# Performance work log

Hardware: AMD Instinct MI355X
Metric: run time of the kernel (lower is better)

Reference implementation:

```python
import jax, jax.numpy as jnp
import numpy as np

PI = 3.141592653589793
EPS = 1e-12  # torch.nn.functional.normalize default eps


def setup_inputs() -> dict:
    key = jax.random.key(0)
    k1, k2, k3, k4 = jax.random.split(key, 4)
    N, D, E, R = 100000, 128, 640000, 500
    z = jax.random.normal(k1, (N, D), dtype=jnp.float32)
    edge_index = jax.random.randint(k2, (2, E), 0, N, dtype=jnp.int64)
    edge_type = jax.random.randint(k3, (E,), 0, R, dtype=jnp.int64)
    # learned relation phases, init uniform(-pi, pi) as in reset_parameters
    phase_rel = jax.random.uniform(k4, (R, D), dtype=jnp.float32, minval=-PI, maxval=PI)
    return {"z": z, "edge_index": edge_index, "edge_type": edge_type, "phase_rel": phase_rel}


def reference(z, edge_index, edge_type, phase_rel):
    # L2-normalize node embeddings along feature dim (torch F.normalize semantics)
    norm = jnp.sqrt(jnp.sum(z * z, axis=1, keepdims=True))
    z = z / jnp.maximum(norm, EPS)
    # z is real (imaginary part zero), rel = exp(i * phase).
    # Re( z_src * rel * conj(z_dst) ) with real z_src, z_dst reduces to
    # z_src * cos(phase) * z_dst  (the sin term multiplies a zero imaginary part).
    z_src = z[edge_index[0]]              # [E, D]
    z_dst = z[edge_index[1]]              # [E, D]
    cos_p = jnp.cos(phase_rel)[edge_type]  # [E, D]
    return jnp.sum(z_src * cos_p * z_dst, axis=1)  # [E]
```

## Files before the change

kernel.cpp:

```cpp
#include <hip/hip_runtime.h>
#include <math.h>

#define D 128
#define EPS_NORM 1e-12f

__device__ __forceinline__ unsigned int f32_to_bf16(float f) {
    unsigned int u = __float_as_uint(f);
    return (u + 0x7FFFu + ((u >> 16) & 1u)) >> 16;
}
__device__ __forceinline__ float bf_lo(unsigned int w) { return __uint_as_float(w << 16); }
__device__ __forceinline__ float bf_hi(unsigned int w) { return __uint_as_float(w & 0xFFFF0000u); }

__global__ void norm_pack_kernel(const float* __restrict__ z,
                                 unsigned int* __restrict__ zn, int N) {
    int w    = blockIdx.x * (blockDim.x >> 6) + (threadIdx.x >> 6);
    int lane = threadIdx.x & 63;
    int half = lane >> 5;
    int hl   = lane & 31;
    int row  = w * 2 + half;
    if (row >= N) return;
    float4 v = reinterpret_cast<const float4*>(z + (size_t)row * D)[hl];
    float s = v.x * v.x + v.y * v.y + v.z * v.z + v.w * v.w;
#pragma unroll
    for (int off = 16; off > 0; off >>= 1) s += __shfl_xor(s, off, 32);
    float inv = 1.0f / fmaxf(sqrtf(s), EPS_NORM);
    uint2 o;
    o.x = (f32_to_bf16(v.y * inv) << 16) | f32_to_bf16(v.x * inv);
    o.y = (f32_to_bf16(v.w * inv) << 16) | f32_to_bf16(v.z * inv);
    reinterpret_cast<uint2*>(zn + (size_t)row * (D / 2))[hl] = o;
}

__global__ void cos_pack_kernel(const float* __restrict__ phase,
                                unsigned int* __restrict__ ct, int n2) {
    int i = blockIdx.x * blockDim.x + threadIdx.x;
    if (i < n2) {
        float a = cosf(phase[2 * i]);
        float b = cosf(phase[2 * i + 1]);
        ct[i] = (f32_to_bf16(b) << 16) | f32_to_bf16(a);
    }
}

__device__ __forceinline__ float dot8(uint4 sw, uint4 cw, uint4 dw) {
    float p;
    p = bf_lo(sw.x) * bf_lo(cw.x) * bf_lo(dw.x);
    p = fmaf(bf_hi(sw.x) * bf_hi(cw.x), bf_hi(dw.x), p);
    p = fmaf(bf_lo(sw.y) * bf_lo(cw.y), bf_lo(dw.y), p);
    p = fmaf(bf_hi(sw.y) * bf_hi(cw.y), bf_hi(dw.y), p);
    p = fmaf(bf_lo(sw.z) * bf_lo(cw.z), bf_lo(dw.z), p);
    p = fmaf(bf_hi(sw.z) * bf_hi(cw.z), bf_hi(dw.z), p);
    p = fmaf(bf_lo(sw.w) * bf_lo(cw.w), bf_lo(dw.w), p);
    p = fmaf(bf_hi(sw.w) * bf_hi(cw.w), bf_hi(dw.w), p);
    return p;
}

__global__ __launch_bounds__(256, 6) void edge_kernel_v4(
    const unsigned int* __restrict__ zn,
    const unsigned int* __restrict__ ct,
    const int* __restrict__ ei,
    const int* __restrict__ et,
    float* __restrict__ out, int E) {
    const uint4* zn4 = reinterpret_cast<const uint4*>(zn);
    const uint4* ct4 = reinterpret_cast<const uint4*>(ct);
    int tid     = (int)(blockIdx.x * blockDim.x + threadIdx.x);
    int gid     = tid >> 4;
    int l       = threadIdx.x & 15;
    int ngroups = (int)((gridDim.x * blockDim.x) >> 4);
    int stride  = ngroups * 4;
    int E4      = E & ~3;

    int e = gid * 4;
    int s0, s1, s2, s3, d0, d1, d2, d3, t0, t1, t2, t3;
    if (e < E4) {
        s0 = ei[e];     s1 = ei[e + 1];     s2 = ei[e + 2];     s3 = ei[e + 3];
        d0 = ei[E + e]; d1 = ei[E + e + 1]; d2 = ei[E + e + 2]; d3 = ei[E + e + 3];
        t0 = et[e];     t1 = et[e + 1];     t2 = et[e + 2];     t3 = et[e + 3];
    }
    for (; e < E4; e += stride) {
        int en = e + stride;
        int ep = (en < E4) ? en : e;
        int ns0 = ei[ep],     ns1 = ei[ep + 1],     ns2 = ei[ep + 2],     ns3 = ei[ep + 3];
        int nd0 = ei[E + ep], nd1 = ei[E + ep + 1], nd2 = ei[E + ep + 2], nd3 = ei[E + ep + 3];
        int nt0 = et[ep],     nt1 = et[ep + 1],     nt2 = et[ep + 2],     nt3 = et[ep + 3];
        uint4 A0 = zn4[(size_t)s0 * 16 + l];
        uint4 B0 = zn4[(size_t)d0 * 16 + l];
        uint4 C0 = ct4[(size_t)t0 * 16 + l];
        uint4 A1 = zn4[(size_t)s1 * 16 + l];
        uint4 B1 = zn4[(size_t)d1 * 16 + l];
        uint4 C1 = ct4[(size_t)t1 * 16 + l];
        uint4 A2 = zn4[(size_t)s2 * 16 + l];
        uint4 B2 = zn4[(size_t)d2 * 16 + l];
        uint4 C2 = ct4[(size_t)t2 * 16 + l];
        uint4 A3 = zn4[(size_t)s3 * 16 + l];
        uint4 B3 = zn4[(size_t)d3 * 16 + l];
        uint4 C3 = ct4[(size_t)t3 * 16 + l];
        float p0 = dot8(A0, C0, B0);
        float p1 = dot8(A1, C1, B1);
        float p2 = dot8(A2, C2, B2);
        float p3 = dot8(A3, C3, B3);
#pragma unroll
        for (int off = 8; off > 0; off >>= 1) {
            p0 += __shfl_xor(p0, off, 64);
            p1 += __shfl_xor(p1, off, 64);
            p2 += __shfl_xor(p2, off, 64);
            p3 += __shfl_xor(p3, off, 64);
        }
        float v = (l == 0) ? p0 : (l == 1) ? p1 : (l == 2) ? p2 : p3;
        if (l < 4) out[e + l] = v;
        s0 = ns0; s1 = ns1; s2 = ns2; s3 = ns3;
        d0 = nd0; d1 = nd1; d2 = nd2; d3 = nd3;
        t0 = nt0; t1 = nt1; t2 = nt2; t3 = nt3;
    }
    for (int e2 = E4 + gid; e2 < E; e2 += ngroups) {
        int s = ei[e2], dd = ei[E + e2], t = et[e2];
        uint4 A = zn4[(size_t)s * 16 + l];
        uint4 B = zn4[(size_t)dd * 16 + l];
        uint4 C = ct4[(size_t)t * 16 + l];
        float p = dot8(A, C, B);
#pragma unroll
        for (int off = 8; off > 0; off >>= 1) p += __shfl_xor(p, off, 64);
        if (l == 0) out[e2] = p;
    }
}

extern "C" void kernel_launch(void* const* d_in, const int* in_sizes, int n_in,
                              void* d_out, int out_size, void* d_ws, size_t ws_size,
                              hipStream_t stream) {
    const float* z          = (const float*)d_in[0];
    const int*   edge_index = (const int*)d_in[1];
    const int*   edge_type  = (const int*)d_in[2];
    const float* phase_rel  = (const float*)d_in[3];
    float* out = (float*)d_out;

    const int N      = in_sizes[0] / D;
    const int E      = in_sizes[2];
    const int nphase = in_sizes[3];

    const size_t zn_bytes = (size_t)N * (D / 2) * sizeof(unsigned int);

    unsigned int* zn = (unsigned int*)d_ws;
    unsigned int* ct = (unsigned int*)((char*)d_ws + zn_bytes);
    (void)ws_size;

    norm_pack_kernel<<<(N + 7) / 8, 256, 0, stream>>>(z, zn, N);

    const int n2 = nphase / 2;
    cos_pack_kernel<<<(n2 + 255) / 256, 256, 0, stream>>>(phase_rel, ct, n2);

    edge_kernel_v4<<<2048, 256, 0, stream>>>(zn, ct, edge_index, edge_type, out, E);
}
```

Before: 62.20 us.

## Merge prep kernels and issue 8-edge batches of gathers per iteration

Fuses the normalize-pack and cosine-pack kernels into one launch, with blocks split by index range, which removes one kernel launch and the gap between launches. The edge kernel now handles 8 edges per group each iteration, issuing all 24 row gathers before any compute, and loads the indices as int4 vectors. The prefetch of the next iteration's indices is dropped. The intent is more memory-level parallelism per wave, paid for with more registers, so launch bounds drop to 4 waves per SIMD. Vector index loads assume 16-byte alignment, which holds because e is a multiple of 8, but ei+E also needs E to be a multiple of 4.

Result: faster. 60.47 us (-2.8%).

```diff
diff --git a/kernel.cpp b/kernel.cpp
--- a/kernel.cpp
+++ b/kernel.cpp
@@ -11,32 +11,32 @@
 __device__ __forceinline__ float bf_lo(unsigned int w) { return __uint_as_float(w << 16); }
 __device__ __forceinline__ float bf_hi(unsigned int w) { return __uint_as_float(w & 0xFFFF0000u); }
 
-__global__ void norm_pack_kernel(const float* __restrict__ z,
-                                 unsigned int* __restrict__ zn, int N) {
-    int w    = blockIdx.x * (blockDim.x >> 6) + (threadIdx.x >> 6);
-    int lane = threadIdx.x & 63;
-    int half = lane >> 5;
-    int hl   = lane & 31;
-    int row  = w * 2 + half;
-    if (row >= N) return;
-    float4 v = reinterpret_cast<const float4*>(z + (size_t)row * D)[hl];
-    float s = v.x * v.x + v.y * v.y + v.z * v.z + v.w * v.w;
+__global__ void prep_kernel(const float* __restrict__ z, unsigned int* __restrict__ zn, int N,
+                            const float* __restrict__ phase, unsigned int* __restrict__ ct, int n2,
+                            int nbz) {
+    if ((int)blockIdx.x < nbz) {
+        int w    = blockIdx.x * 4 + (threadIdx.x >> 6);
+        int lane = threadIdx.x & 63;
+        int half = lane >> 5;
+        int hl   = lane & 31;
+        int row  = w * 2 + half;
+        if (row >= N) return;
+        float4 v = reinterpret_cast<const float4*>(z + (size_t)row * D)[hl];
+        float s = v.x * v.x + v.y * v.y + v.z * v.z + v.w * v.w;
 #pragma unroll
-    for (int off = 16; off > 0; off >>= 1) s += __shfl_xor(s, off, 32);
-    float inv = 1.0f / fmaxf(sqrtf(s), EPS_NORM);
-    uint2 o;
-    o.x = (f32_to_bf16(v.y * inv) << 16) | f32_to_bf16(v.x * inv);
-    o.y = (f32_to_bf16(v.w * inv) << 16) | f32_to_bf16(v.z * inv);
-    reinterpret_cast<uint2*>(zn + (size_t)row * (D / 2))[hl] = o;
-}
-
-__global__ void cos_pack_kernel(const float* __restrict__ phase,
-                                unsigned int* __restrict__ ct, int n2) {
-    int i = blockIdx.x * blockDim.x + threadIdx.x;
-    if (i < n2) {
-        float a = cosf(phase[2 * i]);
-        float b = cosf(phase[2 * i + 1]);
-        ct[i] = (f32_to_bf16(b) << 16) | f32_to_bf16(a);
+        for (int off = 16; off > 0; off >>= 1) s += __shfl_xor(s, off, 32);
+        float inv = 1.0f / fmaxf(sqrtf(s), EPS_NORM);
+        uint2 o;
+        o.x = (f32_to_bf16(v.y * inv) << 16) | f32_to_bf16(v.x * inv);
+        o.y = (f32_to_bf16(v.w * inv) << 16) | f32_to_bf16(v.z * inv);
+        reinterpret_cast<uint2*>(zn + (size_t)row * (D / 2))[hl] = o;
+    } else {
+        int i = (blockIdx.x - nbz) * blockDim.x + threadIdx.x;
+        if (i < n2) {
+            float a = cosf(phase[2 * i]);
+            float b = cosf(phase[2 * i + 1]);
+            ct[i] = (f32_to_bf16(b) << 16) | f32_to_bf16(a);
+        }
     }
 }
 
@@ -53,7 +53,41 @@
     return p;
 }
 
-__global__ __launch_bounds__(256, 6) void edge_kernel_v4(
+#define ISSUE(S, ev)                                                      \
+    int4 S##s = *reinterpret_cast<const int4*>(ei + (ev));                \
+    int4 S##d = *reinterpret_cast<const int4*>(ei + E + (ev));            \
+    int4 S##t = *reinterpret_cast<const int4*>(et + (ev));                \
+    uint4 S##A0 = zn4[(size_t)S##s.x * 16 + l];                           \
+    uint4 S##B0 = zn4[(size_t)S##d.x * 16 + l];                           \
+    uint4 S##C0 = ct4[(size_t)S##t.x * 16 + l];                           \
+    uint4 S##A1 = zn4[(size_t)S##s.y * 16 + l];                           \
+    uint4 S##B1 = zn4[(size_t)S##d.y * 16 + l];                           \
+    uint4 S##C1 = ct4[(size_t)S##t.y * 16 + l];                           \
+    uint4 S##A2 = zn4[(size_t)S##s.z * 16 + l];                           \
+    uint4 S##B2 = zn4[(size_t)S##d.z * 16 + l];                           \
+    uint4 S##C2 = ct4[(size_t)S##t.z * 16 + l];                           \
+    uint4 S##A3 = zn4[(size_t)S##s.w * 16 + l];                           \
+    uint4 S##B3 = zn4[(size_t)S##d.w * 16 + l];                           \
+    uint4 S##C3 = ct4[(size_t)S##t.w * 16 + l];
+
+#define COMPUTE(S, ebase)                                                 \
+    {                                                                     \
+        float p0 = dot8(S##A0, S##C0, S##B0);                             \
+        float p1 = dot8(S##A1, S##C1, S##B1);                             \
+        float p2 = dot8(S##A2, S##C2, S##B2);                             \
+        float p3 = dot8(S##A3, S##C3, S##B3);                             \
+        _Pragma("unroll")                                                 \
+        for (int off = 8; off > 0; off >>= 1) {                           \
+            p0 += __shfl_xor(p0, off, 64);                                \
+            p1 += __shfl_xor(p1, off, 64);                                \
+            p2 += __shfl_xor(p2, off, 64);                                \
+            p3 += __shfl_xor(p3, off, 64);                                \
+        }                                                                 \
+        float v = (l == 0) ? p0 : (l == 1) ? p1 : (l == 2) ? p2 : p3;     \
+        if (l < 4) out[(ebase) + l] = v;                                  \
+    }
+
+__global__ __launch_bounds__(256, 4) void edge_kernel_v5(
     const unsigned int* __restrict__ zn,
     const unsigned int* __restrict__ ct,
     const int* __restrict__ ei,
@@ -65,52 +99,17 @@
     int gid     = tid >> 4;
     int l       = threadIdx.x & 15;
     int ngroups = (int)((gridDim.x * blockDim.x) >> 4);
-    int stride  = ngroups * 4;
-    int E4      = E & ~3;
+    int stride  = ngroups * 8;
+    int E8      = E & ~7;
 
-    int e = gid * 4;
-    int s0, s1, s2, s3, d0, d1, d2, d3, t0, t1, t2, t3;
-    if (e < E4) {
-        s0 = ei[e];     s1 = ei[e + 1];     s2 = ei[e + 2];     s3 = ei[e + 3];
-        d0 = ei[E + e]; d1 = ei[E + e + 1]; d2 = ei[E + e + 2]; d3 = ei[E + e + 3];
-        t0 = et[e];     t1 = et[e + 1];     t2 = et[e + 2];     t3 = et[e + 3];
+    for (int e = gid * 8; e + 8 <= E8; e += stride) {
+        ISSUE(P, e)
+        ISSUE(Q, e + 4)
+        asm volatile("" ::: "memory");
+        COMPUTE(P, e)
+        COMPUTE(Q, e + 4)
     }
-    for (; e < E4; e += stride) {
-        int en = e + stride;
-        int ep = (en < E4) ? en : e;
-        int ns0 = ei[ep],     ns1 = ei[ep + 1],     ns2 = ei[ep + 2],     ns3 = ei[ep + 3];
-        int nd0 = ei[E + ep], nd1 = ei[E + ep + 1], nd2 = ei[E + ep + 2], nd3 = ei[E + ep + 3];
-        int nt0 = et[ep],     nt1 = et[ep + 1],     nt2 = et[ep + 2],     nt3 = et[ep + 3];
-        uint4 A0 = zn4[(size_t)s0 * 16 + l];
-        uint4 B0 = zn4[(size_t)d0 * 16 + l];
-        uint4 C0 = ct4[(size_t)t0 * 16 + l];
-        uint4 A1 = zn4[(size_t)s1 * 16 + l];
-        uint4 B1 = zn4[(size_t)d1 * 16 + l];
-        uint4 C1 = ct4[(size_t)t1 * 16 + l];
-        uint4 A2 = zn4[(size_t)s2 * 16 + l];
-        uint4 B2 = zn4[(size_t)d2 * 16 + l];
-        uint4 C2 = ct4[(size_t)t2 * 16 + l];
-        uint4 A3 = zn4[(size_t)s3 * 16 + l];
-        uint4 B3 = zn4[(size_t)d3 * 16 + l];
-        uint4 C3 = ct4[(size_t)t3 * 16 + l];
-        float p0 = dot8(A0, C0, B0);
-        float p1 = dot8(A1, C1, B1);
-        float p2 = dot8(A2, C2, B2);
-        float p3 = dot8(A3, C3, B3);
-#pragma unroll
-        for (int off = 8; off > 0; off >>= 1) {
-            p0 += __shfl_xor(p0, off, 64);
-            p1 += __shfl_xor(p1, off, 64);
-            p2 += __shfl_xor(p2, off, 64);
-            p3 += __shfl_xor(p3, off, 64);
-        }
-        float v = (l == 0) ? p0 : (l == 1) ? p1 : (l == 2) ? p2 : p3;
-        if (l < 4) out[e + l] = v;
-        s0 = ns0; s1 = ns1; s2 = ns2; s3 = ns3;
-        d0 = nd0; d1 = nd1; d2 = nd2; d3 = nd3;
-        t0 = nt0; t1 = nt1; t2 = nt2; t3 = nt3;
-    }
-    for (int e2 = E4 + gid; e2 < E; e2 += ngroups) {
+    for (int e2 = E8 + gid; e2 < E; e2 += ngroups) {
         int s = ei[e2], dd = ei[E + e2], t = et[e2];
         uint4 A = zn4[(size_t)s * 16 + l];
         uint4 B = zn4[(size_t)dd * 16 + l];
@@ -141,10 +140,10 @@
     unsigned int* ct = (unsigned int*)((char*)d_ws + zn_bytes);
     (void)ws_size;
 
-    norm_pack_kernel<<<(N + 7) / 8, 256, 0, stream>>>(z, zn, N);
+    const int n2  = nphase / 2;
+    const int nbz = (N + 7) / 8;
+    const int nbc = (n2 + 255) / 256;
+    prep_kernel<<<nbz + nbc, 256, 0, stream>>>(z, zn, N, phase_rel, ct, n2, nbz);
 
-    const int n2 = nphase / 2;
-    cos_pack_kernel<<<(n2 + 255) / 256, 256, 0, stream>>>(phase_rel, ct, n2);
-
-    edge_kernel_v4<<<2048, 256, 0, stream>>>(zn, ct, edge_index, edge_type, out, E);
+    edge_kernel_v5<<<2048, 256, 0, stream>>>(zn, ct, edge_index, edge_type, out, E);
 }
```
